# Optimization experiments

Hardware: AMD Instinct MI355X
Metric: run time of the kernel (lower is better)

## Reference

```python
import jax, jax.numpy as jnp
import numpy as np

N, D, NUM_CLASSES = 8192, 1024, 128
ALPHA = 0.1
EPS = 1e-7


def setup_inputs() -> dict:
    key = jax.random.key(0)
    k1, k2 = jax.random.split(key)
    H = jax.random.normal(k1, (N, D), dtype=jnp.float32)
    labels = jax.random.randint(k2, (N,), 0, NUM_CLASSES, dtype=jnp.int64)
    return {"H": H, "labels": labels}


def reference(H, labels):
    n = H.shape[0]
    # squared-euclidean pairwise distances: ||x_i - x_j||^2
    x_norm = jnp.sum(H * H, axis=1)                      # [N]
    dists = x_norm[:, None] + x_norm[None, :] - 2.0 * (H @ H.T)
    dists = jnp.where(jnp.isnan(dists), 0.0, dists)      # dist[dist != dist] = 0
    dists = jnp.maximum(dists, 0.0)                      # clamp(0, inf)
    dists = jnp.maximum(dists, EPS)                      # clamp(min=1e-7)

    diffs = labels[None, :] - labels[:, None]            # [N, N]
    eye = jnp.eye(n, dtype=bool)
    mask_pos = (diffs == 0) & ~eye                       # same label, not self
    mask_neg = diffs != 0                                # different label

    # hardest positive: argmax over positive-masked distances
    anchor_positive_dist = jnp.where(mask_pos, dists, 0.0)
    hardest_positive_idx = jnp.argmax(anchor_positive_dist, axis=1)

    # hard negative: add row-max to non-negatives, take 2nd-smallest (k=1 partition)
    max_neg = jnp.max(dists, axis=1, keepdims=True)
    anchor_negative_dist = dists + max_neg * (1.0 - mask_neg.astype(dists.dtype))
    _, idx2 = jax.lax.top_k(-anchor_negative_dist, 2)    # two smallest per row
    hardest_negatives_idx = idx2[:, 1]

    rows = jnp.arange(n)
    hardest_positive_dist = dists[rows, hardest_positive_idx]
    hardest_negative_dist = dists[rows, hardest_negatives_idx]
    differences = hardest_positive_dist - hardest_negative_dist

    triplet_loss = jnp.maximum(differences + ALPHA, 0.0)  # final='plus', do_max=True
    relevant = triplet_loss > EPS                          # boolean mask (no grad)
    count = jnp.sum(relevant.astype(triplet_loss.dtype))
    return jnp.sum(jnp.where(relevant, triplet_loss, 0.0)) / count
```

## Files before the change

### kernel.cpp

```cpp
#include <hip/hip_runtime.h>
#include <hip/hip_bf16.h>
#include <stdint.h>

constexpr int Nn = 8192;
constexpr int Dd = 1024;
constexpr float kAlpha = 0.1f;
constexpr float kEps = 1e-7f;
constexpr float kInf = 3.0e38f;

constexpr int BM = 128, BN = 128, BK = 32;
constexpr int NB = Nn / BM;
constexpr int NPAIR = NB * (NB + 1) / 2;

constexpr int TILE_SH = 4096;

using bfx8 = __attribute__((ext_vector_type(8))) __bf16;
using f32x4 = __attribute__((ext_vector_type(4))) float;

__device__ __forceinline__ unsigned short f2bf(float f) {
  union { float f; unsigned int u; } v; v.f = f;
  unsigned int u = v.u;
  u = u + 0x7fffu + ((u >> 16) & 1u);
  return (unsigned short)(u >> 16);
}

__device__ __forceinline__ void min2_insert(float& m1, float& m2, float x) {
  const float lo = fminf(m1, x);
  const float hi = fmaxf(m1, x);
  m1 = lo;
  m2 = fminf(m2, hi);
}

__device__ __forceinline__ void min2_merge(float& m1, float& m2, float o1, float o2) {
  m2 = fminf(fminf(m2, o2), fmaxf(m1, o1));
  m1 = fminf(m1, o1);
}

__global__ __launch_bounds__(256) void prep_kernel(const float* __restrict__ H,
                                                   unsigned short* __restrict__ Hb,
                                                   float* __restrict__ xn) {
  const int wave = threadIdx.x >> 6;
  const int lane = threadIdx.x & 63;
  const int row = blockIdx.x * 4 + wave;
  const float4* src = (const float4*)(H + (size_t)row * Dd);
  unsigned short* dstBase =
      Hb + ((size_t)(row >> 7) * 32) * TILE_SH + (row & 127) * 32;
  float acc = 0.f;
#pragma unroll
  for (int i = 0; i < 4; ++i) {
    float4 v = src[lane + 64 * i];
    acc = fmaf(v.x, v.x, acc);
    acc = fmaf(v.y, v.y, acc);
    acc = fmaf(v.z, v.z, acc);
    acc = fmaf(v.w, v.w, acc);
    ushort4 o;
    o.x = f2bf(v.x); o.y = f2bf(v.y); o.z = f2bf(v.z); o.w = f2bf(v.w);
    const int k4 = (lane + 64 * i) * 4;
    *(ushort4*)(dstBase + (k4 >> 5) * TILE_SH + (k4 & 31)) = o;
  }
#pragma unroll
  for (int off = 32; off; off >>= 1) acc += __shfl_xor(acc, off, 64);
  if (lane == 0) xn[row] = acc;
}

__global__ __launch_bounds__(256, 3) void triplet_main(
    const unsigned short* __restrict__ Hb, const float* __restrict__ xn,
    const int* __restrict__ lab, float* __restrict__ wsMax,
    float* __restrict__ wsM1, float* __restrict__ wsM2) {
  __shared__ __align__(16) unsigned char smem[32768];

  const int tid = threadIdx.x;
  const int wave = tid >> 6;
  const int lane = tid & 63;
  const int quad = lane >> 4;
  const int l15 = lane & 15;
  const int wm = wave & 1;
  const int wn = wave >> 1;

  int bid = (int)blockIdx.x;
  bid = (bid & 7) * (NPAIR / 8) + (bid >> 3);

  int b = bid, I = 0;
  while (b >= NB - I) { b -= NB - I; ++I; }
  const int J = I + b;
  const bool diag = (I == J);

  const int rowBase = I * BM;
  const int colBase = J * BN;

  int lr[16]; float xr[16];
#pragma unroll
  for (int m = 0; m < 4; ++m)
#pragma unroll
    for (int r = 0; r < 4; ++r) {
      const int row = rowBase + wm * 64 + m * 16 + quad * 4 + r;
      lr[m * 4 + r] = lab[row];
      xr[m * 4 + r] = xn[row];
    }

  float maxp[16], mn1[16], mn2[16];
#pragma unroll
  for (int s = 0; s < 16; ++s) { maxp[s] = 0.f; mn1[s] = kInf; mn2[s] = kInf; }

  const int stR = lane >> 2;
  const int stRow = wave * 32 + stR;
  const int stCol = ((lane & 3) ^ ((stR >> 1) & 3)) * 8;
  const int swq = quad ^ ((l15 >> 1) & 3);

  f32x4 acc[4][4];
#pragma unroll
  for (int m = 0; m < 4; ++m)
#pragma unroll
    for (int n = 0; n < 4; ++n) acc[m][n] = {0.f, 0.f, 0.f, 0.f};

  auto stage = [&](int bsel, int kti) {
    unsigned short* As = (unsigned short*)(smem + bsel * 16384);
    unsigned short* Bs = (unsigned short*)(smem + bsel * 16384 + 8192);
    const unsigned short* baseA = Hb + (size_t)(I * 32 + kti) * TILE_SH;
    const unsigned short* baseB = Hb + (size_t)(J * 32 + kti) * TILE_SH;
#pragma unroll
    for (int j = 0; j < 2; ++j) {
      const unsigned short* ga = baseA + (stRow + j * 16) * 32 + stCol;
      __builtin_amdgcn_global_load_lds(
          (const __attribute__((address_space(1))) void*)ga,
          (__attribute__((address_space(3))) void*)&As[(wave * 2 + j) * 512],
          16, 0, 0);
      const unsigned short* gb = baseB + (stRow + j * 16) * 32 + stCol;
      __builtin_amdgcn_global_load_lds(
          (const __attribute__((address_space(1))) void*)gb,
          (__attribute__((address_space(3))) void*)&Bs[(wave * 2 + j) * 512],
          16, 0, 0);
    }
  };

  stage(0, 0);
  __syncthreads();

  int cur = 0;
  for (int kti = 0; kti < Dd / BK; ++kti) {
    if (kti + 1 < Dd / BK) stage(cur ^ 1, kti + 1);

    const unsigned short* As = (const unsigned short*)(smem + cur * 16384);
    const unsigned short* Bs = (const unsigned short*)(smem + cur * 16384 + 8192);
    bfx8 a[4], bb[4];
#pragma unroll
    for (int m = 0; m < 4; ++m)
      a[m] = *(const bfx8*)&As[(wm * 64 + m * 16 + l15) * BK + swq * 8];
#pragma unroll
    for (int n = 0; n < 4; ++n)
      bb[n] = *(const bfx8*)&Bs[(wn * 64 + n * 16 + l15) * BK + swq * 8];
#pragma unroll
    for (int m = 0; m < 4; ++m)
#pragma unroll
      for (int n = 0; n < 4; ++n)
        acc[m][n] = __builtin_amdgcn_mfma_f32_16x16x32_bf16(a[m], bb[n], acc[m][n], 0, 0, 0);

    __syncthreads();
    cur ^= 1;
  }

  int lc[4]; float xc[4];
#pragma unroll
  for (int n = 0; n < 4; ++n) {
    const int col = colBase + wn * 64 + n * 16 + l15;
    lc[n] = lab[col];
    xc[n] = xn[col];
  }
  float tmaxp[4], tmn1[4], tmn2[4];
#pragma unroll
  for (int n = 0; n < 4; ++n) { tmaxp[n] = 0.f; tmn1[n] = kInf; tmn2[n] = kInf; }

  if (!diag) {
#pragma unroll
    for (int m = 0; m < 4; ++m)
#pragma unroll
      for (int n = 0; n < 4; ++n)
#pragma unroll
        for (int r = 0; r < 4; ++r) {
          const int s = m * 4 + r;
          const float d = fmaf(-2.f, acc[m][n][r], xr[s] + xc[n]);
          const bool eq = (lr[s] == lc[n]);
          const float pos = eq ? d : 0.f;
          const float dn = eq ? kInf : d;
          maxp[s] = fmaxf(maxp[s], pos);
          min2_insert(mn1[s], mn2[s], dn);
          tmaxp[n] = fmaxf(tmaxp[n], pos);
          min2_insert(tmn1[n], tmn2[n], dn);
        }
  } else {
#pragma unroll
    for (int m = 0; m < 4; ++m)
#pragma unroll
      for (int n = 0; n < 4; ++n)
#pragma unroll
        for (int r = 0; r < 4; ++r) {
          const int s = m * 4 + r;
          const bool selfp = (wm == wn) && (m == n) && (quad * 4 + r == l15);
          const float d = fmaf(-2.f, acc[m][n][r], xr[s] + xc[n]);
          const bool eq = (lr[s] == lc[n]);
          const float pos = (eq && !selfp) ? d : 0.f;
          const float dn = eq ? kInf : d;
          maxp[s] = fmaxf(maxp[s], pos);
          min2_insert(mn1[s], mn2[s], dn);
        }
  }

#pragma unroll
  for (int off = 1; off < 16; off <<= 1) {
#pragma unroll
    for (int s = 0; s < 16; ++s) {
      const float om = __shfl_xor(maxp[s], off, 64);
      const float o1 = __shfl_xor(mn1[s], off, 64);
      const float o2 = __shfl_xor(mn2[s], off, 64);
      maxp[s] = fmaxf(maxp[s], om);
      min2_merge(mn1[s], mn2[s], o1, o2);
    }
  }

  float* rbuf = (float*)smem;
  float* tbm = ((float*)smem) + 384;
  float* tb1 = tbm + 1024;
  float* tb2 = tb1 + 1024;

  if (wn == 1 && l15 == 0) {
#pragma unroll
    for (int m = 0; m < 4; ++m)
#pragma unroll
      for (int r = 0; r < 4; ++r) {
        const int s = m * 4 + r;
        const int local = m * 16 + quad * 4 + r;
        rbuf[(wm * 64 + local) * 3 + 0] = maxp[s];
        rbuf[(wm * 64 + local) * 3 + 1] = mn1[s];
        rbuf[(wm * 64 + local) * 3 + 2] = mn2[s];
      }
  }
#pragma unroll
  for (int n = 0; n < 4; ++n) {
    const int idx = (((wm * 2 + wn) * 4 + quad) * 4 + n) * 16 + l15;
    tbm[idx] = tmaxp[n];
    tb1[idx] = tmn1[n];
    tb2[idx] = tmn2[n];
  }
  __syncthreads();

  if (wn == 0 && l15 == 0) {
#pragma unroll
    for (int m = 0; m < 4; ++m)
#pragma unroll
      for (int r = 0; r < 4; ++r) {
        const int s = m * 4 + r;
        const int local = m * 16 + quad * 4 + r;
        float om = rbuf[(wm * 64 + local) * 3 + 0];
        float o1 = rbuf[(wm * 64 + local) * 3 + 1];
        float o2 = rbuf[(wm * 64 + local) * 3 + 2];
        const float M = fmaxf(maxp[s], om);
        float a1 = mn1[s], a2 = mn2[s];
        min2_merge(a1, a2, o1, o2);
        const size_t p = ((size_t)(I * NB + J)) * 128 + wm * 64 + local;
        wsMax[p] = M;
        wsM1[p] = a1;
        wsM2[p] = a2;
      }
  }
  if (wm == 0 && !diag) {
    const int tn = lane >> 4;
    const int tl = lane & 15;
    float M = 0.f, a1 = kInf, a2 = kInf;
#pragma unroll
    for (int wm2 = 0; wm2 < 2; ++wm2)
#pragma unroll
      for (int q = 0; q < 4; ++q) {
        const int idx = (((wm2 * 2 + wn) * 4 + q) * 4 + tn) * 16 + tl;
        M = fmaxf(M, tbm[idx]);
        min2_merge(a1, a2, tb1[idx], tb2[idx]);
      }
    const size_t p = ((size_t)(J * NB + I)) * 128 + wn * 64 + lane;
    wsMax[p] = M;
    wsM1[p] = a1;
    wsM2[p] = a2;
  }
}

__global__ __launch_bounds__(256) void merge_kernel(
    const float* __restrict__ wsMax, const float* __restrict__ wsM1,
    const float* __restrict__ wsM2, float* __restrict__ bsum,
    float* __restrict__ bcnt) {
  const int r = threadIdx.x & 127;
  const int h = threadIdx.x >> 7;
  const int bi = blockIdx.x;
  float mp = 0.f, m1 = kInf, m2 = kInf;
#pragma unroll 8
  for (int bj = h * 32; bj < h * 32 + 32; ++bj) {
    const size_t p = ((size_t)(bi * NB + bj)) * 128 + r;
    mp = fmaxf(mp, wsMax[p]);
    min2_merge(m1, m2, wsM1[p], wsM2[p]);
  }
  __shared__ float hmax[128], hm1[128], hm2[128];
  if (h == 1) { hmax[r] = mp; hm1[r] = m1; hm2[r] = m2; }
  __syncthreads();
  float ls = 0.f, lc = 0.f;
  if (h == 0) {
    mp = fmaxf(mp, hmax[r]);
    min2_merge(m1, m2, hm1[r], hm2[r]);
    const float loss = fmaxf(mp - m2 + kAlpha, 0.f);
    ls = (loss > kEps) ? loss : 0.f;
    lc = (loss > kEps) ? 1.f : 0.f;
  }
#pragma unroll
  for (int off = 32; off; off >>= 1) {
    ls += __shfl_down(ls, off, 64);
    lc += __shfl_down(lc, off, 64);
  }
  __shared__ float ss[2], sc[2];
  if (h == 0 && (threadIdx.x & 63) == 0) {
    ss[threadIdx.x >> 6] = ls;
    sc[threadIdx.x >> 6] = lc;
  }
  __syncthreads();
  if (threadIdx.x == 0) {
    bsum[bi] = ss[0] + ss[1];
    bcnt[bi] = sc[0] + sc[1];
  }
}

__global__ __launch_bounds__(64) void final_kernel(const float* __restrict__ bsum,
                                                   const float* __restrict__ bcnt,
                                                   float* __restrict__ out) {
  float s = bsum[threadIdx.x];
  float c = bcnt[threadIdx.x];
#pragma unroll
  for (int off = 32; off; off >>= 1) {
    s += __shfl_down(s, off, 64);
    c += __shfl_down(c, off, 64);
  }
  if (threadIdx.x == 0) out[0] = s / c;
}

extern "C" void kernel_launch(void* const* d_in, const int* in_sizes, int n_in,
                              void* d_out, int out_size, void* d_ws, size_t ws_size,
                              hipStream_t stream) {
  (void)in_sizes; (void)n_in; (void)out_size; (void)ws_size;
  const float* H = (const float*)d_in[0];
  const int* lab = (const int*)d_in[1];
  float* out = (float*)d_out;

  char* ws = (char*)d_ws;
  unsigned short* Hb = (unsigned short*)ws;
  float* xn = (float*)(ws + (size_t)Nn * Dd * sizeof(unsigned short));
  float* wsMax = xn + Nn;
  float* wsM1 = wsMax + NB * NB * 128;
  float* wsM2 = wsM1 + NB * NB * 128;
  float* bsum = wsM2 + NB * NB * 128;
  float* bcnt = bsum + NB;

  prep_kernel<<<Nn / 4, 256, 0, stream>>>(H, Hb, xn);
  triplet_main<<<NPAIR, 256, 0, stream>>>(Hb, xn, lab, wsMax, wsM1, wsM2);
  merge_kernel<<<NB, 256, 0, stream>>>(wsMax, wsM1, wsM2, bsum, bcnt);
  final_kernel<<<1, 64, 0, stream>>>(bsum, bcnt, out);
}
```

Measured before the change: 183.5 us.

## Restructure epilogue per m-block to cut registers and raise occupancy to 4

Drops the 16-entry per-thread row label, norm and reduction arrays that stayed live through the GEMM loop. The epilogue now loads row data and reduces one m-block at a time, writes both column-warp partials to LDS, and lets 128 threads merge and store the row results. This lowers register pressure so launch_bounds can ask for 4 blocks per SM instead of 3. The cost is more shuffle and LDS rounds and possible spills if the register cap is tight.

```diff
diff --git a/kernel.cpp b/kernel.cpp
--- a/kernel.cpp
+++ b/kernel.cpp
@@ -11,6 +11,7 @@
 constexpr int BM = 128, BN = 128, BK = 32;
 constexpr int NB = Nn / BM;
 constexpr int NPAIR = NB * (NB + 1) / 2;
+constexpr int NT = Dd / BK;
 
 constexpr int TILE_SH = 4096;
 
@@ -63,7 +64,7 @@
   if (lane == 0) xn[row] = acc;
 }
 
-__global__ __launch_bounds__(256, 3) void triplet_main(
+__global__ __launch_bounds__(256, 4) void triplet_main(
     const unsigned short* __restrict__ Hb, const float* __restrict__ xn,
     const int* __restrict__ lab, float* __restrict__ wsMax,
     float* __restrict__ wsM1, float* __restrict__ wsM2) {
@@ -87,20 +88,6 @@
 
   const int rowBase = I * BM;
   const int colBase = J * BN;
-
-  int lr[16]; float xr[16];
-#pragma unroll
-  for (int m = 0; m < 4; ++m)
-#pragma unroll
-    for (int r = 0; r < 4; ++r) {
-      const int row = rowBase + wm * 64 + m * 16 + quad * 4 + r;
-      lr[m * 4 + r] = lab[row];
-      xr[m * 4 + r] = xn[row];
-    }
-
-  float maxp[16], mn1[16], mn2[16];
-#pragma unroll
-  for (int s = 0; s < 16; ++s) { maxp[s] = 0.f; mn1[s] = kInf; mn2[s] = kInf; }
 
   const int stR = lane >> 2;
   const int stRow = wave * 32 + stR;
@@ -137,8 +124,8 @@
   __syncthreads();
 
   int cur = 0;
-  for (int kti = 0; kti < Dd / BK; ++kti) {
-    if (kti + 1 < Dd / BK) stage(cur ^ 1, kti + 1);
+  for (int kti = 0; kti < NT; ++kti) {
+    if (kti + 1 < NT) stage(cur ^ 1, kti + 1);
 
     const unsigned short* As = (const unsigned short*)(smem + cur * 16384);
     const unsigned short* Bs = (const unsigned short*)(smem + cur * 16384 + 8192);
@@ -158,6 +145,11 @@
     __syncthreads();
     cur ^= 1;
   }
+
+  float* rbuf = (float*)smem;
+  float* tbm = ((float*)smem) + 768;
+  float* tb1 = tbm + 1024;
+  float* tb2 = tb1 + 1024;
 
   int lc[4]; float xc[4];
 #pragma unroll
@@ -170,70 +162,70 @@
 #pragma unroll
   for (int n = 0; n < 4; ++n) { tmaxp[n] = 0.f; tmn1[n] = kInf; tmn2[n] = kInf; }
 
-  if (!diag) {
-#pragma unroll
-    for (int m = 0; m < 4; ++m)
+#pragma unroll
+  for (int m = 0; m < 4; ++m) {
+    int lr4[4]; float xr4[4];
+#pragma unroll
+    for (int r = 0; r < 4; ++r) {
+      const int row = rowBase + wm * 64 + m * 16 + quad * 4 + r;
+      lr4[r] = lab[row];
+      xr4[r] = xn[row];
+    }
+    float rmax[4], r1v[4], r2v[4];
+#pragma unroll
+    for (int r = 0; r < 4; ++r) { rmax[r] = 0.f; r1v[r] = kInf; r2v[r] = kInf; }
+
+    if (!diag) {
 #pragma unroll
       for (int n = 0; n < 4; ++n)
 #pragma unroll
         for (int r = 0; r < 4; ++r) {
-          const int s = m * 4 + r;
-          const float d = fmaf(-2.f, acc[m][n][r], xr[s] + xc[n]);
-          const bool eq = (lr[s] == lc[n]);
+          const float d = fmaf(-2.f, acc[m][n][r], xr4[r] + xc[n]);
+          const bool eq = (lr4[r] == lc[n]);
           const float pos = eq ? d : 0.f;
           const float dn = eq ? kInf : d;
-          maxp[s] = fmaxf(maxp[s], pos);
-          min2_insert(mn1[s], mn2[s], dn);
+          rmax[r] = fmaxf(rmax[r], pos);
+          min2_insert(r1v[r], r2v[r], dn);
           tmaxp[n] = fmaxf(tmaxp[n], pos);
           min2_insert(tmn1[n], tmn2[n], dn);
         }
-  } else {
-#pragma unroll
-    for (int m = 0; m < 4; ++m)
+    } else {
 #pragma unroll
       for (int n = 0; n < 4; ++n)
 #pragma unroll
         for (int r = 0; r < 4; ++r) {
-          const int s = m * 4 + r;
           const bool selfp = (wm == wn) && (m == n) && (quad * 4 + r == l15);
-          const float d = fmaf(-2.f, acc[m][n][r], xr[s] + xc[n]);
-          const bool eq = (lr[s] == lc[n]);
+          const float d = fmaf(-2.f, acc[m][n][r], xr4[r] + xc[n]);
+          const bool eq = (lr4[r] == lc[n]);
           const float pos = (eq && !selfp) ? d : 0.f;
           const float dn = eq ? kInf : d;
-          maxp[s] = fmaxf(maxp[s], pos);
-          min2_insert(mn1[s], mn2[s], dn);
+          rmax[r] = fmaxf(rmax[r], pos);
+          min2_insert(r1v[r], r2v[r], dn);
         }
-  }
-
-#pragma unroll
-  for (int off = 1; off < 16; off <<= 1) {
-#pragma unroll
-    for (int s = 0; s < 16; ++s) {
-      const float om = __shfl_xor(maxp[s], off, 64);
-      const float o1 = __shfl_xor(mn1[s], off, 64);
-      const float o2 = __shfl_xor(mn2[s], off, 64);
-      maxp[s] = fmaxf(maxp[s], om);
-      min2_merge(mn1[s], mn2[s], o1, o2);
-    }
-  }
-
-  float* rbuf = (float*)smem;
-  float* tbm = ((float*)smem) + 384;
-  float* tb1 = tbm + 1024;
-  float* tb2 = tb1 + 1024;
-
-  if (wn == 1 && l15 == 0) {
-#pragma unroll
-    for (int m = 0; m < 4; ++m)
+    }
+
+#pragma unroll
+    for (int off = 1; off < 16; off <<= 1) {
 #pragma unroll
       for (int r = 0; r < 4; ++r) {
-        const int s = m * 4 + r;
-        const int local = m * 16 + quad * 4 + r;
-        rbuf[(wm * 64 + local) * 3 + 0] = maxp[s];
-        rbuf[(wm * 64 + local) * 3 + 1] = mn1[s];
-        rbuf[(wm * 64 + local) * 3 + 2] = mn2[s];
+        const float om = __shfl_xor(rmax[r], off, 64);
+        const float o1 = __shfl_xor(r1v[r], off, 64);
+        const float o2 = __shfl_xor(r2v[r], off, 64);
+        rmax[r] = fmaxf(rmax[r], om);
+        min2_merge(r1v[r], r2v[r], o1, o2);
       }
-  }
+    }
+    if (l15 == 0) {
+#pragma unroll
+      for (int r = 0; r < 4; ++r) {
+        const int row = wm * 64 + m * 16 + quad * 4 + r;
+        rbuf[(wn * 128 + row) * 3 + 0] = rmax[r];
+        rbuf[(wn * 128 + row) * 3 + 1] = r1v[r];
+        rbuf[(wn * 128 + row) * 3 + 2] = r2v[r];
+      }
+    }
+  }
+
 #pragma unroll
   for (int n = 0; n < 4; ++n) {
     const int idx = (((wm * 2 + wn) * 4 + quad) * 4 + n) * 16 + l15;
@@ -243,24 +235,15 @@
   }
   __syncthreads();
 
-  if (wn == 0 && l15 == 0) {
-#pragma unroll
-    for (int m = 0; m < 4; ++m)
-#pragma unroll
-      for (int r = 0; r < 4; ++r) {
-        const int s = m * 4 + r;
-        const int local = m * 16 + quad * 4 + r;
-        float om = rbuf[(wm * 64 + local) * 3 + 0];
-        float o1 = rbuf[(wm * 64 + local) * 3 + 1];
-        float o2 = rbuf[(wm * 64 + local) * 3 + 2];
-        const float M = fmaxf(maxp[s], om);
-        float a1 = mn1[s], a2 = mn2[s];
-        min2_merge(a1, a2, o1, o2);
-        const size_t p = ((size_t)(I * NB + J)) * 128 + wm * 64 + local;
-        wsMax[p] = M;
-        wsM1[p] = a1;
-        wsM2[p] = a2;
-      }
+  if (tid < 128) {
+    const int row = tid;
+    float M = fmaxf(rbuf[row * 3 + 0], rbuf[(128 + row) * 3 + 0]);
+    float a1 = rbuf[row * 3 + 1], a2 = rbuf[row * 3 + 2];
+    min2_merge(a1, a2, rbuf[(128 + row) * 3 + 1], rbuf[(128 + row) * 3 + 2]);
+    const size_t p = ((size_t)(I * NB + J)) * 128 + row;
+    wsMax[p] = M;
+    wsM1[p] = a1;
+    wsM2[p] = a2;
   }
   if (wm == 0 && !diag) {
     const int tn = lane >> 4;
```

New measurement: 177.7 us. 1.03x faster.
